# Performance work log

Hardware: AMD Instinct MI355X
Metric: run time of the kernel (lower is better)

## Reference

```python
import jax, jax.numpy as jnp
import numpy as np

B, V, C, M, CM, D, OUT = 16, 16, 64, 32, 16, 128, 600
VOCAB = {"cond": 4000, "proc": 2000, "drug": 600, "lab_item": 700, "lab_value": 2000, "inj_item": 400, "inj_value": 2000}


def _gru(x, Wih, Whh, bih, bhh):
    """Batch-first torch-style GRU. x: [N,T,D] -> (outputs [N,T,D], h_T [N,D])."""
    Dh = Whh.shape[1]

    def step(h, xt):
        gi = xt @ Wih.T + bih
        gh = h @ Whh.T + bhh
        ir, iz, ig = jnp.split(gi, 3, axis=-1)
        hr, hz, hg = jnp.split(gh, 3, axis=-1)
        r = jax.nn.sigmoid(ir + hr)
        z = jax.nn.sigmoid(iz + hz)
        n = jnp.tanh(ig + r * hg)
        h = (1.0 - z) * n + z * h
        return h, h

    h0 = jnp.zeros((x.shape[0], Dh), x.dtype)
    hT, ys = jax.lax.scan(step, h0, jnp.swapaxes(x, 0, 1))
    return jnp.swapaxes(ys, 0, 1), hT


def _hetero_mp(feats, Wself, Wmsg):
    """Heterogeneous message passing over node types on the fully-connected
    monitor<->visit-feature bipartite pattern: each node type combines a self
    transform with a transformed mean of the other node types, then ReLU.
    feats: list of [N,D]; Wself/Wmsg: [T,D,D]."""
    stacked = jnp.stack(feats)  # [T,N,D]
    total = jnp.sum(stacked, axis=0)
    T = stacked.shape[0]
    outs = []
    for t in range(T):
        others = (total - stacked[t]) / (T - 1)
        outs.append(jax.nn.relu(stacked[t] @ Wself[t] + others @ Wmsg[t]))
    return outs


def _forward(codes_cond, codes_proc, codes_drug, codes_lab_item, codes_lab_value,
             codes_inj_item, codes_inj_value, weight, age,
             emb_cond, emb_proc, emb_drug, emb_lab_item, emb_lab_value,
             emb_inj_item, emb_inj_value,
             mgru_Wih, mgru_Whh, mgru_bih, mgru_bhh,
             vgru_Wih, vgru_Whh, vgru_bih, vgru_bhh,
             gnn_Wself, gnn_Wmsg,
             fc_weight_W, fc_weight_b, fc_age_W, fc_age_b,
             fc_patient_W, fc_patient_b):
    # ---- visit-event features: embedding lookup + sum-pool over codes ----
    vis = {}
    for k, codes, emb in (("cond", codes_cond, emb_cond),
                          ("proc", codes_proc, emb_proc),
                          ("drug", codes_drug, emb_drug)):
        vis[k] = jnp.sum(emb[codes], axis=2)  # [B,V,D]
    visit_keys = ("cond", "proc", "drug")

    # ---- monitor-event pairs: (item * value) embeddings, GNN, two-level GRU ----
    pairs = (
        (codes_lab_item, codes_lab_value, emb_lab_item, emb_lab_value, "lab_item", (0, 2, 3, 4)),
        (codes_inj_item, codes_inj_value, emb_inj_item, emb_inj_value, "inj_item", (1, 2, 3, 4)),
    )
    hid = {}
    for p, (ci, cv, ei, ev, ikey, gidx) in enumerate(pairs):
        mon = jnp.sum(ei[ci] * ev[cv], axis=3)  # [B,V,M,D]
        feats = [mon.reshape(-1, D)]  # monitor node type, [B*V*M, D]
        for k in visit_keys:  # visit features repeated across monitors
            feats.append(jnp.broadcast_to(vis[k][:, :, None, :], (B, V, M, D)).reshape(-1, D))
        outs = _hetero_mp(feats, gnn_Wself[p], gnn_Wmsg[p])
        for t, k in enumerate((ikey,) + visit_keys):
            g = gidx[t]
            # monitor-level GRU over the M monitors of each visit
            o, _ = _gru(outs[t].reshape(B * V, M, D), mgru_Wih[g], mgru_Whh[g], mgru_bih[g], mgru_bhh[g])
            last = o[:, -1, :].reshape(B, V, D)  # last monitor state per visit
            # visit-level GRU (source uses visit_gru[feature_key1] for all keys)
            _, h = _gru(last, vgru_Wih[p], vgru_Whh[p], vgru_bih[p], vgru_bhh[p])
            hid[k] = h if k not in hid else hid[k] + h

    # ---- weight / age scalar features ----
    for k, x, W, b, vi in (("weight", weight, fc_weight_W, fc_weight_b, 2),
                           ("age", age, fc_age_W, fc_age_b, 3)):
        mask = (x != 0.0)[..., None]  # [B,V,1]
        xe = (x[..., None] * W[:, 0] + b) * mask  # Linear(1->D) then zero-mask
        _, h = _gru(xe, vgru_Wih[vi], vgru_Whh[vi], vgru_bih[vi], vgru_bhh[vi])
        hid[k] = h

    # ---- concat in dict-insertion order, then ReLU + Linear head ----
    pe = jnp.concatenate([hid["lab_item"], hid["cond"], hid["proc"], hid["drug"],
                          hid["inj_item"], hid["weight"], hid["age"]], axis=-1)  # [B, 7D]
    return jax.nn.relu(pe) @ fc_patient_W.T + fc_patient_b  # [B, OUT]


def setup_inputs() -> dict:
    key = jax.random.key(0)
    ks = iter(jax.random.split(key, 64))

    def nrm(shape, s=0.1):
        return (jax.random.normal(next(ks), shape) * s).astype(jnp.float32)

    def emb_table(vsz):
        t = nrm((vsz, D), 1.0)
        return t.at[0].set(0.0)  # padding_idx=0 row is zero

    inp = {}
    inp["codes_cond"] = jax.random.randint(next(ks), (B, V, C), 0, VOCAB["cond"], dtype=jnp.int32)
    inp["codes_proc"] = jax.random.randint(next(ks), (B, V, C), 0, VOCAB["proc"], dtype=jnp.int32)
    inp["codes_drug"] = jax.random.randint(next(ks), (B, V, C), 0, VOCAB["drug"], dtype=jnp.int32)
    inp["codes_lab_item"] = jax.random.randint(next(ks), (B, V, M, CM), 0, VOCAB["lab_item"], dtype=jnp.int32)
    inp["codes_lab_value"] = jax.random.randint(next(ks), (B, V, M, CM), 0, VOCAB["lab_value"], dtype=jnp.int32)
    inp["codes_inj_item"] = jax.random.randint(next(ks), (B, V, M, CM), 0, VOCAB["inj_item"], dtype=jnp.int32)
    inp["codes_inj_value"] = jax.random.randint(next(ks), (B, V, M, CM), 0, VOCAB["inj_value"], dtype=jnp.int32)
    inp["weight"] = jax.random.uniform(next(ks), (B, V), minval=0.1, maxval=1.0, dtype=jnp.float32)
    inp["age"] = jax.random.uniform(next(ks), (B, V), minval=0.1, maxval=1.0, dtype=jnp.float32)
    inp["emb_cond"] = emb_table(VOCAB["cond"])
    inp["emb_proc"] = emb_table(VOCAB["proc"])
    inp["emb_drug"] = emb_table(VOCAB["drug"])
    inp["emb_lab_item"] = emb_table(VOCAB["lab_item"])
    inp["emb_lab_value"] = emb_table(VOCAB["lab_value"])
    inp["emb_inj_item"] = emb_table(VOCAB["inj_item"])
    inp["emb_inj_value"] = emb_table(VOCAB["inj_value"])
    inp["mgru_Wih"] = nrm((5, 3 * D, D))
    inp["mgru_Whh"] = nrm((5, 3 * D, D))
    inp["mgru_bih"] = nrm((5, 3 * D))
    inp["mgru_bhh"] = nrm((5, 3 * D))
    inp["vgru_Wih"] = nrm((4, 3 * D, D))
    inp["vgru_Whh"] = nrm((4, 3 * D, D))
    inp["vgru_bih"] = nrm((4, 3 * D))
    inp["vgru_bhh"] = nrm((4, 3 * D))
    inp["gnn_Wself"] = nrm((2, 4, D, D))
    inp["gnn_Wmsg"] = nrm((2, 4, D, D))
    inp["fc_weight_W"] = nrm((D, 1))
    inp["fc_weight_b"] = nrm((D,))
    inp["fc_age_W"] = nrm((D, 1))
    inp["fc_age_b"] = nrm((D,))
    inp["fc_patient_W"] = nrm((OUT, 7 * D))
    inp["fc_patient_b"] = nrm((OUT,))
    return inp


def reference(codes_cond, codes_proc, codes_drug, codes_lab_item, codes_lab_value,
              codes_inj_item, codes_inj_value, weight, age,
              emb_cond, emb_proc, emb_drug, emb_lab_item, emb_lab_value,
              emb_inj_item, emb_inj_value,
              mgru_Wih, mgru_Whh, mgru_bih, mgru_bhh,
              vgru_Wih, vgru_Whh, vgru_bih, vgru_bhh,
              gnn_Wself, gnn_Wmsg,
              fc_weight_W, fc_weight_b, fc_age_W, fc_age_b,
              fc_patient_W, fc_patient_b):
    return _forward(codes_cond, codes_proc, codes_drug, codes_lab_item, codes_lab_value,
                    codes_inj_item, codes_inj_value, weight, age,
                    emb_cond, emb_proc, emb_drug, emb_lab_item, emb_lab_value,
                    emb_inj_item, emb_inj_value,
                    mgru_Wih, mgru_Whh, mgru_bih, mgru_bhh,
                    vgru_Wih, vgru_Whh, vgru_bih, vgru_bhh,
                    gnn_Wself, gnn_Wmsg,
                    fc_weight_W, fc_weight_b, fc_age_W, fc_age_b,
                    fc_patient_W, fc_patient_b)
```

## Files before the change

### kernel.cpp

```cpp
#include <hip/hip_runtime.h>
#include <math.h>

#define B_   16
#define V_   16
#define C_   64
#define M_   32
#define CM_  16
#define D_   128
#define OUT_ 600
#define NSEQ 256
#define NROW 8192

typedef __attribute__((ext_vector_type(8))) short bf16x8;
typedef __attribute__((ext_vector_type(4))) short bf16x4;
typedef __attribute__((ext_vector_type(4))) float f32x4;

__device__ __forceinline__ unsigned short f2bf(float x) {
  union { float f; unsigned u; } v; v.f = x;
  unsigned r = v.u + 0x7fff + ((v.u >> 16) & 1);
  return (unsigned short)(r >> 16);
}
__device__ __forceinline__ float bf2f(short s) {
  union { unsigned u; float f; } v;
  v.u = ((unsigned)(unsigned short)s) << 16;
  return v.f;
}
__device__ __forceinline__ float fsig(float x)  { return __fdividef(1.f, 1.f + __expf(-x)); }
__device__ __forceinline__ float ftanh(float x) { return 1.f - 2.f*__fdividef(1.f, __expf(2.f*x) + 1.f); }

constexpr int OFF_VIS   = 0;
constexpr int OFF_VISB  = 98304;
constexpr int OFF_MONB  = 147456;
constexpr int OFF_TOTB  = 1196032;
constexpr int OFF_W12T  = 2244608;
constexpr int OFF_WIHB  = 2375680;
constexpr int OFF_WIHTV = 2498560;
constexpr int OFF_XE    = 2695168;
constexpr int OFF_GI    = 2760704;
constexpr int OFF_LAST  = 27926528;
constexpr int OFF_VH    = 29171712;

__global__ __launch_bounds__(256) void k_prepvis(
    const float* __restrict__ Wself, const float* __restrict__ Wmsg,
    const float* __restrict__ mWih,  const float* __restrict__ vWih,
    const float* __restrict__ wgt,   const float* __restrict__ age,
    const float* __restrict__ fwW,   const float* __restrict__ fwB,
    const float* __restrict__ faW,   const float* __restrict__ faB,
    const int* __restrict__ cc, const int* __restrict__ cp, const int* __restrict__ cd,
    const float* __restrict__ ec, const float* __restrict__ ep, const float* __restrict__ ed,
    short* __restrict__ w12t, short* __restrict__ wihb,
    float* __restrict__ wihTv, float* __restrict__ xe,
    float* __restrict__ vis, short* __restrict__ visb)
{
  int bx = blockIdx.x, tid = threadIdx.x;
  if (bx < 1024) {
    int lin = bx*256 + tid;
    int pt = lin >> 15, rem = lin & 32767;
    int n = rem >> 8, k = rem & 255;
    float v;
    if (k < 128) v = Wself[pt*16384 + k*128 + n] - Wmsg[pt*16384 + k*128 + n]*(1.f/3.f);
    else         v = Wmsg[pt*16384 + (k-128)*128 + n]*(1.f/3.f);
    w12t[lin] = (short)f2bf(v);
  } else if (bx < 1984) {
    int lin = (bx-1024)*256 + tid;
    wihb[lin] = (short)f2bf(mWih[lin]);
  } else if (bx < 2752) {
    int lin = (bx-1984)*256 + tid;
    int g = lin / 49152, rem2 = lin % 49152;
    int k = rem2 / 384, j = rem2 % 384;
    wihTv[lin] = vWih[g*49152 + j*128 + k];
  } else if (bx < 3008) {
    int lin = (bx-2752)*256 + tid;
    int which = lin >> 15, rem2 = lin & 32767;
    int n = rem2 >> 7, d = rem2 & 127;
    float x  = which ? age[n] : wgt[n];
    float Wv = which ? faW[d] : fwW[d];
    float bb = which ? faB[d] : fwB[d];
    xe[lin] = (x != 0.0f) ? (x*Wv + bb) : 0.0f;
  } else {
    int idx = (bx-3008)*256 + tid;
    int type = idx >> 15;
    int r = idx & 32767;
    int bv = r >> 7, d = r & 127;
    const int*   codes = (type==0) ? cc : (type==1) ? cp : cd;
    const float* emb   = (type==0) ? ec : (type==1) ? ep : ed;
    float acc = 0.f;
    for (int c = 0; c < C_; ++c) {
      int code = codes[bv*C_ + c];
      acc += emb[code*D_ + d];
    }
    vis [(type*NSEQ + bv)*D_ + d] = acc;
    visb[(type*NSEQ + bv)*D_ + d] = (short)f2bf(acc);
  }
}

__global__ __launch_bounds__(128) void k_mon(
    const int* __restrict__ cli, const int* __restrict__ clv,
    const int* __restrict__ cii, const int* __restrict__ civ,
    const float* __restrict__ eli, const float* __restrict__ elv,
    const float* __restrict__ eii, const float* __restrict__ eiv,
    const float* __restrict__ vis,
    short* __restrict__ monb, short* __restrict__ totb)
{
  int p   = blockIdx.x >> 13;
  int bvm = blockIdx.x & 8191;
  int d   = threadIdx.x;
  const int* ci = p ? cii : cli;  const int* cv = p ? civ : clv;
  const float* ei = p ? eii : eli; const float* ev = p ? eiv : elv;
  float acc = 0.f;
  #pragma unroll
  for (int c = 0; c < CM_; ++c) {
    int iv = ci[bvm*CM_ + c];
    int vv = cv[bvm*CM_ + c];
    acc += ei[iv*D_ + d] * ev[vv*D_ + d];
  }
  int bv = bvm >> 5;
  float vsum = vis[bv*D_ + d] + vis[(NSEQ + bv)*D_ + d] + vis[(2*NSEQ + bv)*D_ + d];
  monb[(p*NROW + bvm)*D_ + d] = (short)f2bf(acc);
  totb[(p*NROW + bvm)*D_ + d] = (short)f2bf(acc + vsum);
}

__global__ __launch_bounds__(256, 4) void k_gg(
    const short* __restrict__ monb, const short* __restrict__ totb,
    const short* __restrict__ visb, const short* __restrict__ w12t,
    const short* __restrict__ wihb, const float* __restrict__ mbih,
    short* __restrict__ gi)
{
  const int pt = blockIdx.x >> 6;
  const int rb = blockIdx.x & 63;
  const int p = pt >> 2, t = pt & 3;
  const int g = (pt % 4 == 0) ? (pt / 4) : (pt % 4 + 1);
  const int row0 = rb * 128;
  const int tid = threadIdx.x;
  const int w = tid >> 6, lane = tid & 63;
  const int c = lane & 15, q = lane >> 4;

  __shared__ short smem[2*128*72];
  short (*Xs)[72]  = (short(*)[72])smem;
  short (*Ws)[72]  = (short(*)[72])(smem + 128*72);
  short (*Ys)[136] = (short(*)[136])smem;
  float (*giS)[68] = (float(*)[68])smem;

  const int rowL = tid >> 1, kc = tid & 1;
  const int rowG = row0 + rowL;
  const int bv = rowG >> 5;
  const int mg = w >> 1, ng = w & 1;

  f32x4 acc1[4][4];
  #pragma unroll
  for (int mi = 0; mi < 4; ++mi)
    #pragma unroll
    for (int ni = 0; ni < 4; ++ni) acc1[mi][ni] = (f32x4){0.f,0.f,0.f,0.f};

  const short* featp = (t == 0) ? (monb + ((size_t)p*NROW + rowG)*128)
                                : (visb + ((size_t)(t-1)*NSEQ + bv)*128);
  const short* totp  = totb + ((size_t)p*NROW + rowG)*128;
  const short* wrow  = w12t + ((size_t)pt*128 + rowL)*256;

  #pragma unroll 1
  for (int ks = 0; ks < 4; ++ks) {
    __syncthreads();
    int kg = ks*64 + kc*32;
    const short* srcX = (kg < 128) ? (featp + kg) : (totp + (kg - 128));
    const short* srcW = wrow + kg;
    short* dX = &Xs[rowL][kc*32];
    short* dW = &Ws[rowL][kc*32];
    #pragma unroll
    for (int i = 0; i < 4; ++i) {
      *(bf16x8*)(dX + 8*i) = *(const bf16x8*)(srcX + 8*i);
      *(bf16x8*)(dW + 8*i) = *(const bf16x8*)(srcW + 8*i);
    }
    __syncthreads();
    #pragma unroll
    for (int kk = 0; kk < 2; ++kk) {
      bf16x8 af[4], bfr[4];
      #pragma unroll
      for (int mi = 0; mi < 4; ++mi)
        af[mi] = *(const bf16x8*)&Xs[(mg*4+mi)*16 + c][kk*32 + q*8];
      #pragma unroll
      for (int ni = 0; ni < 4; ++ni)
        bfr[ni] = *(const bf16x8*)&Ws[(ng*4+ni)*16 + c][kk*32 + q*8];
      #pragma unroll
      for (int mi = 0; mi < 4; ++mi)
        #pragma unroll
        for (int ni = 0; ni < 4; ++ni)
          acc1[mi][ni] = __builtin_amdgcn_mfma_f32_16x16x32_bf16(af[mi], bfr[ni], acc1[mi][ni], 0, 0, 0);
    }
  }
  __syncthreads();

  #pragma unroll
  for (int mi = 0; mi < 4; ++mi)
    #pragma unroll
    for (int ni = 0; ni < 4; ++ni)
      #pragma unroll
      for (int reg = 0; reg < 4; ++reg)
        Ys[(mg*4+mi)*16 + q*4 + reg][(ng*4+ni)*16 + c] =
            (short)f2bf(fmaxf(acc1[mi][ni][reg], 0.f));
  __syncthreads();

  bf16x8 Af[2][4];
  #pragma unroll
  for (int mi = 0; mi < 2; ++mi)
    #pragma unroll
    for (int kt = 0; kt < 4; ++kt)
      Af[mi][kt] = *(const bf16x8*)&Ys[(w*2+mi)*16 + c][kt*32 + q*8];

  float bihv[24];
  #pragma unroll
  for (int nt = 0; nt < 24; ++nt)
    bihv[nt] = mbih[g*384 + nt*16 + c];

  short* gslab = gi + (((size_t)pt*64 + rb)*32)*384*4;
  #pragma unroll 1
  for (int cn = 0; cn < 6; ++cn) {
    f32x4 acc2[2][4];
    #pragma unroll
    for (int mi = 0; mi < 2; ++mi)
      #pragma unroll
      for (int ni = 0; ni < 4; ++ni) acc2[mi][ni] = (f32x4){0.f,0.f,0.f,0.f};
    #pragma unroll
    for (int ni = 0; ni < 4; ++ni) {
      int n = (cn*4 + ni)*16 + c;
      const short* bp_ = wihb + ((size_t)g*384 + n)*128 + q*8;
      #pragma unroll
      for (int kt = 0; kt < 4; ++kt) {
        bf16x8 bfr = *(const bf16x8*)(bp_ + kt*32);
        #pragma unroll
        for (int mi = 0; mi < 2; ++mi)
          acc2[mi][ni] = __builtin_amdgcn_mfma_f32_16x16x32_bf16(Af[mi][kt], bfr, acc2[mi][ni], 0, 0, 0);
      }
    }
    __syncthreads();
    #pragma unroll
    for (int mi = 0; mi < 2; ++mi)
      #pragma unroll
      for (int ni = 0; ni < 4; ++ni) {
        float bia = bihv[cn*4+ni];
        #pragma unroll
        for (int reg = 0; reg < 4; ++reg)
          giS[(w*2+mi)*16 + q*4 + reg][ni*16 + c] = acc2[mi][ni][reg] + bia;
      }
    __syncthreads();
    #pragma unroll
    for (int k = 0; k < 8; ++k) {
      int o4 = tid + k*256;
      int m = o4 >> 6, colL = o4 & 63;
      bf16x4 v;
      v[0] = (short)f2bf(giS[m][colL]);
      v[1] = (short)f2bf(giS[32+m][colL]);
      v[2] = (short)f2bf(giS[64+m][colL]);
      v[3] = (short)f2bf(giS[96+m][colL]);
      *(bf16x4*)&gslab[((size_t)m*384 + cn*64 + colL)*4] = v;
    }
  }
}

__global__ __launch_bounds__(512, 1) void k_mgru(
    const short* __restrict__ gi, const float* __restrict__ mWhh,
    const float* __restrict__ mbhh, float* __restrict__ last)
{
  const int run = blockIdx.x >> 5, grp = blockIdx.x & 31;
  const int g = (run % 4 == 0) ? (run / 4) : (run % 4 + 1);
  const int tid = threadIdx.x;
  const int w = tid >> 6;
  const int lane = tid & 63;
  const int c = lane & 15, q = lane >> 4;

  __shared__ short hb[2][4][16][40];
  for (int idx = tid; idx < 2*4*16*40; idx += 512)
    ((short*)hb)[idx] = 0;

  const int jh = w*16 + c;

  bf16x8 bfrag[3][4];
  #pragma unroll
  for (int gate = 0; gate < 3; ++gate) {
    const float* wp = mWhh + ((size_t)g*384 + gate*128 + jh)*128 + q*8;
    #pragma unroll
    for (int kt = 0; kt < 4; ++kt) {
      float4 lo = *(const float4*)(wp + kt*32);
      float4 hi = *(const float4*)(wp + kt*32 + 4);
      bf16x8 t;
      t[0]=(short)f2bf(lo.x); t[1]=(short)f2bf(lo.y); t[2]=(short)f2bf(lo.z); t[3]=(short)f2bf(lo.w);
      t[4]=(short)f2bf(hi.x); t[5]=(short)f2bf(hi.y); t[6]=(short)f2bf(hi.z); t[7]=(short)f2bf(hi.w);
      bfrag[gate][kt] = t;
    }
  }
  float bh_[3];
  #pragma unroll
  for (int gate = 0; gate < 3; ++gate)
    bh_[gate] = mbhh[g*384 + gate*128 + jh];

  float hf[4] = {0.f,0.f,0.f,0.f};
  const short* gib = gi + (((size_t)run*64 + grp*2 + q)*32)*384*4;
  const bool act = (lane < 32);

  bf16x4 gA[3], gB[3];
  if (act) {
    #pragma unroll
    for (int gate = 0; gate < 3; ++gate)
      gA[gate] = *(const bf16x4*)&gib[(size_t)(0*384 + gate*128 + jh)*4];
  }
  __syncthreads();

  auto dostep = [&](int m, bf16x4 (&gcur)[3], bf16x4 (&gnext)[3]) {
    const int cur = m & 1, nxt = cur ^ 1;
    bf16x8 a[4];
    #pragma unroll
    for (int kt = 0; kt < 4; ++kt)
      a[kt] = *(const bf16x8*)&hb[cur][kt][c][q*8];

    f32x4 acc[3];
    #pragma unroll
    for (int gate = 0; gate < 3; ++gate) {
      f32x4 t = {0.f,0.f,0.f,0.f};
      #pragma unroll
      for (int kt = 0; kt < 4; ++kt)
        t = __builtin_amdgcn_mfma_f32_16x16x32_bf16(a[kt], bfrag[gate][kt], t, 0, 0, 0);
      acc[gate] = t;
    }

    if (act && m < 31) {
      #pragma unroll
      for (int gate = 0; gate < 3; ++gate)
        gnext[gate] = *(const bf16x4*)&gib[(size_t)((m+1)*384 + gate*128 + jh)*4];
    }

    if (act) {
      const int kt = jh >> 5, kk = jh & 31;
      #pragma unroll
      for (int reg = 0; reg < 4; ++reg) {
        int row = q*4 + reg;
        float g0 = bf2f(gcur[0][reg]);
        float g1 = bf2f(gcur[1][reg]);
        float g2 = bf2f(gcur[2][reg]);
        float rr = fsig(acc[0][reg] + bh_[0] + g0);
        float zz = fsig(acc[1][reg] + bh_[1] + g1);
        float nn = ftanh(g2 + rr*(acc[2][reg] + bh_[2]));
        float hnew = (1.f - zz)*nn + zz*hf[reg];
        hf[reg] = hnew;
        hb[nxt][kt][row][kk] = (short)f2bf(hnew);
      }
    }
    __syncthreads();
  };

  #pragma unroll 1
  for (int m2 = 0; m2 < 16; ++m2) {
    dostep(2*m2,     gA, gB);
    dostep(2*m2 + 1, gB, gA);
  }

  if (act) {
    #pragma unroll
    for (int reg = 0; reg < 4; ++reg)
      last[(run*NSEQ + grp*8 + q*4 + reg)*D_ + jh] = hf[reg];
  }
}

__global__ __launch_bounds__(768) void k_vgru(
    const float* __restrict__ last, const float* __restrict__ xe,
    const float* __restrict__ wihTv, const float* __restrict__ vbih,
    const float* __restrict__ vWhh, const float* __restrict__ vbhh,
    float* __restrict__ vh)
{
  int run = blockIdx.x >> 4, b = blockIdx.x & 15;
  int tid = threadIdx.x;
  int vidx = (run < 4) ? 0 : (run < 8) ? 1 : (run - 6);

  __shared__ float Xs[16][128];
  __shared__ float giL[16*384];
  __shared__ __align__(16) float hsv[128];
  __shared__ float gh[384];

  const float* X = (run < 8) ? (last + ((size_t)run*NSEQ + b*16)*D_)
                             : (xe + ((size_t)(run-8)*NSEQ + b*16)*D_);
  for (int idx = tid; idx < 2048; idx += 768)
    ((float*)Xs)[idx] = X[idx];
  if (tid < 128) hsv[tid] = 0.f;
  __syncthreads();

  {
    int half = (tid >= 384) ? 1 : 0;
    int j = tid - half*384;
    float accv[8];
    float bias = vbih[vidx*384 + j];
    #pragma unroll
    for (int s = 0; s < 8; ++s) accv[s] = bias;
    const float* W = wihTv + vidx*49152 + j;
    #pragma unroll 4
    for (int k = 0; k < 128; ++k) {
      float wv = W[k*384];
      #pragma unroll
      for (int s = 0; s < 8; ++s) accv[s] += Xs[half*8 + s][k] * wv;
    }
    #pragma unroll
    for (int s = 0; s < 8; ++s)
      giL[(half*8 + s)*384 + j] = accv[s];
  }

  int j = tid >> 1, kh = tid & 1;
  float w[64];
  const float4* wrow = (const float4*)(vWhh + (vidx*384 + j)*128 + kh*64);
  #pragma unroll
  for (int k4 = 0; k4 < 16; ++k4) {
    float4 t4 = wrow[k4];
    w[4*k4] = t4.x; w[4*k4+1] = t4.y; w[4*k4+2] = t4.z; w[4*k4+3] = t4.w;
  }
  float bj = vbhh[vidx*384 + j];
  __syncthreads();

  #pragma unroll 1
  for (int v = 0; v < 16; ++v) {
    const float4* h4 = (const float4*)(hsv + kh*64);
    float p0 = 0.f, p1 = 0.f;
    #pragma unroll
    for (int k4 = 0; k4 < 8; ++k4) {
      float4 u0 = h4[k4], u1 = h4[k4+8];
      p0 += w[4*k4   ]*u0.x + w[4*k4+1 ]*u0.y + w[4*k4+2 ]*u0.z + w[4*k4+3 ]*u0.w;
      p1 += w[4*k4+32]*u1.x + w[4*k4+33]*u1.y + w[4*k4+34]*u1.z + w[4*k4+35]*u1.w;
    }
    float part = p0 + p1;
    part += __shfl_xor(part, 1);
    if (kh == 0) gh[j] = bj + ((j < 256) ? giL[v*384 + j] : 0.f) + part;
    __syncthreads();
    if (tid < 128) {
      float r = fsig(gh[tid]);
      float z = fsig(gh[tid+128]);
      float gin = giL[v*384 + 256 + tid];
      float n = ftanh(gin + r*gh[tid+256]);
      hsv[tid] = (1.f - z)*n + z*hsv[tid];
    }
    __syncthreads();
  }
  if (tid < 128) vh[(run*16 + b)*D_ + tid] = hsv[tid];
}

__global__ __launch_bounds__(256) void k_head(
    const float* __restrict__ vh, const float* __restrict__ Wp,
    const float* __restrict__ bp, float* __restrict__ out)
{
  const int o = blockIdx.x;
  const int tid = threadIdx.x;
  const int b = tid & 15, kc = tid >> 4;
  const int a1[7] = {0,1,2,3,4,8,9};
  const int a2[7] = {-1,5,6,7,-1,-1,-1};
  const float4* wb = (const float4*)(Wp + (size_t)o*896 + kc*56);
  float acc = 0.f;
  #pragma unroll
  for (int i = 0; i < 14; ++i) {
    int cc2 = kc*56 + i*4;
    int s = cc2 >> 7, d0 = cc2 & 127;
    float4 a = *(const float4*)(vh + (a1[s]*16 + b)*D_ + d0);
    int s2 = a2[s];
    if (s2 >= 0) {
      float4 a2v = *(const float4*)(vh + (s2*16 + b)*D_ + d0);
      a.x += a2v.x; a.y += a2v.y; a.z += a2v.z; a.w += a2v.w;
    }
    a.x = fmaxf(a.x, 0.f); a.y = fmaxf(a.y, 0.f);
    a.z = fmaxf(a.z, 0.f); a.w = fmaxf(a.w, 0.f);
    float4 ww = wb[i];
    acc += a.x*ww.x + a.y*ww.y + a.z*ww.z + a.w*ww.w;
  }
  __shared__ float red[16][17];
  red[kc][b] = acc;
  __syncthreads();
  if (tid < 16) {
    float s = 0.f;
    #pragma unroll
    for (int k = 0; k < 16; ++k) s += red[k][tid];
    out[tid*OUT_ + o] = s + bp[o];
  }
}

extern "C" void kernel_launch(void* const* d_in, const int* in_sizes, int n_in,
                              void* d_out, int out_size, void* d_ws, size_t ws_size,
                              hipStream_t stream)
{
  (void)in_sizes; (void)n_in; (void)out_size; (void)ws_size;
  const int*   cc   = (const int*)  d_in[0];
  const int*   cp   = (const int*)  d_in[1];
  const int*   cd   = (const int*)  d_in[2];
  const int*   cli  = (const int*)  d_in[3];
  const int*   clv  = (const int*)  d_in[4];
  const int*   cii  = (const int*)  d_in[5];
  const int*   civ  = (const int*)  d_in[6];
  const float* wgt  = (const float*)d_in[7];
  const float* age  = (const float*)d_in[8];
  const float* ec   = (const float*)d_in[9];
  const float* ep   = (const float*)d_in[10];
  const float* ed   = (const float*)d_in[11];
  const float* eli  = (const float*)d_in[12];
  const float* elv  = (const float*)d_in[13];
  const float* eii  = (const float*)d_in[14];
  const float* eiv  = (const float*)d_in[15];
  const float* mWih = (const float*)d_in[16];
  const float* mWhh = (const float*)d_in[17];
  const float* mbih = (const float*)d_in[18];
  const float* mbhh = (const float*)d_in[19];
  const float* vWih = (const float*)d_in[20];
  const float* vWhh = (const float*)d_in[21];
  const float* vbih = (const float*)d_in[22];
  const float* vbhh = (const float*)d_in[23];
  const float* Wself= (const float*)d_in[24];
  const float* Wmsg = (const float*)d_in[25];
  const float* fwW  = (const float*)d_in[26];
  const float* fwB  = (const float*)d_in[27];
  const float* faW  = (const float*)d_in[28];
  const float* faB  = (const float*)d_in[29];
  const float* Wp   = (const float*)d_in[30];
  const float* bp   = (const float*)d_in[31];
  float* out = (float*)d_out;
  float* ws  = (float*)d_ws;

  float* vis   = ws + OFF_VIS;
  short* visb  = (short*)(ws + OFF_VISB);
  short* monb  = (short*)(ws + OFF_MONB);
  short* totb  = (short*)(ws + OFF_TOTB);
  short* w12t  = (short*)(ws + OFF_W12T);
  short* wihb  = (short*)(ws + OFF_WIHB);
  float* wihTv = ws + OFF_WIHTV;
  float* xe    = ws + OFF_XE;
  short* gi    = (short*)(ws + OFF_GI);
  float* last  = ws + OFF_LAST;
  float* vh    = ws + OFF_VH;

  k_prepvis<<<3392, 256, 0, stream>>>(Wself, Wmsg, mWih, vWih, wgt, age,
                                      fwW, fwB, faW, faB,
                                      cc, cp, cd, ec, ep, ed,
                                      w12t, wihb, wihTv, xe, vis, visb);
  k_mon <<<16384, 128, 0, stream>>>(cli, clv, cii, civ, eli, elv, eii, eiv,
                                    vis, monb, totb);
  k_gg  <<<512, 256, 0, stream>>>(monb, totb, visb, w12t, wihb, mbih, gi);
  k_mgru<<<256, 512, 0, stream>>>(gi, mWhh, mbhh, last);
  k_vgru<<<160, 768, 0, stream>>>(last, xe, wihTv, vbih, vWhh, vbhh, vh);
  k_head<<<600, 256, 0, stream>>>(vh, Wp, bp, out);
}
```

Baseline: 279.7 us.

## Restructure monitor GRU to split MFMA and gate math across 1024-thread blocks

Result: no change. 280.8 us (+0.4%).

```diff
diff --git a/kernel.cpp b/kernel.cpp
--- a/kernel.cpp
+++ b/kernel.cpp
@@ -24,6 +24,9 @@
   union { unsigned u; float f; } v;
   v.u = ((unsigned)(unsigned short)s) << 16;
   return v.f;
+}
+__device__ __forceinline__ float u2f(unsigned u) {
+  union { unsigned u; float f; } v; v.u = u; return v.f;
 }
 __device__ __forceinline__ float fsig(float x)  { return __fdividef(1.f, 1.f + __expf(-x)); }
 __device__ __forceinline__ float ftanh(float x) { return 1.f - 2.f*__fdividef(1.f, __expf(2.f*x) + 1.f); }
@@ -256,11 +259,12 @@
   }
 }
 
-__global__ __launch_bounds__(512, 1) void k_mgru(
+__global__ __launch_bounds__(1024) void k_mgru(
     const short* __restrict__ gi, const float* __restrict__ mWhh,
     const float* __restrict__ mbhh, float* __restrict__ last)
 {
-  const int run = blockIdx.x >> 5, grp = blockIdx.x & 31;
+  const int run  = blockIdx.x >> 4;
+  const int pair = blockIdx.x & 15;
   const int g = (run % 4 == 0) ? (run / 4) : (run % 4 + 1);
   const int tid = threadIdx.x;
   const int w = tid >> 6;
@@ -268,95 +272,104 @@
   const int c = lane & 15, q = lane >> 4;
 
   __shared__ short hb[2][4][16][40];
-  for (int idx = tid; idx < 2*4*16*40; idx += 512)
+  __shared__ float gS[384][20];
+
+  for (int idx = tid; idx < 2*4*16*40; idx += 1024)
     ((short*)hb)[idx] = 0;
 
-  const int jh = w*16 + c;
-
-  bf16x8 bfrag[3][4];
-  #pragma unroll
-  for (int gate = 0; gate < 3; ++gate) {
-    const float* wp = mWhh + ((size_t)g*384 + gate*128 + jh)*128 + q*8;
-    #pragma unroll
-    for (int kt = 0; kt < 4; ++kt) {
-      float4 lo = *(const float4*)(wp + kt*32);
-      float4 hi = *(const float4*)(wp + kt*32 + 4);
-      bf16x8 t;
-      t[0]=(short)f2bf(lo.x); t[1]=(short)f2bf(lo.y); t[2]=(short)f2bf(lo.z); t[3]=(short)f2bf(lo.w);
-      t[4]=(short)f2bf(hi.x); t[5]=(short)f2bf(hi.y); t[6]=(short)f2bf(hi.z); t[7]=(short)f2bf(hi.w);
-      bfrag[gate][kt] = t;
-    }
-  }
-  float bh_[3];
+  const bool mfw = (w < 12);
+  const int gate_w = w >> 2;
+  const int nt = w & 3;
+  bf16x8 bfrag[2][4];
+  if (mfw) {
+    #pragma unroll
+    for (int ti = 0; ti < 2; ++ti) {
+      const int col = gate_w*128 + nt*32 + ti*16 + c;
+      const float* wp = mWhh + ((size_t)g*384 + col)*128 + q*8;
+      #pragma unroll
+      for (int kt = 0; kt < 4; ++kt) {
+        float4 lo = *(const float4*)(wp + kt*32);
+        float4 hi = *(const float4*)(wp + kt*32 + 4);
+        bf16x8 tt;
+        tt[0]=(short)f2bf(lo.x); tt[1]=(short)f2bf(lo.y); tt[2]=(short)f2bf(lo.z); tt[3]=(short)f2bf(lo.w);
+        tt[4]=(short)f2bf(hi.x); tt[5]=(short)f2bf(hi.y); tt[6]=(short)f2bf(hi.z); tt[7]=(short)f2bf(hi.w);
+        bfrag[ti][kt] = tt;
+      }
+    }
+  }
+
+  const int j  = tid >> 3;
+  const int sp = tid & 7;
+  const int s0 = sp*2;
+  const int ktj = j >> 5, kkj = j & 31;
+  const float bh0 = mbhh[g*384 +       j];
+  const float bh1 = mbhh[g*384 + 128 + j];
+  const float bh2 = mbhh[g*384 + 256 + j];
+  const short* gip = gi + (((size_t)run*64 + pair*4 + (s0>>2))*32)*384*4
+                        + (size_t)j*4 + (s0&3);
+
+  float h0 = 0.f, h1 = 0.f;
+
+  unsigned gA[3], gB[3];
   #pragma unroll
   for (int gate = 0; gate < 3; ++gate)
-    bh_[gate] = mbhh[g*384 + gate*128 + jh];
-
-  float hf[4] = {0.f,0.f,0.f,0.f};
-  const short* gib = gi + (((size_t)run*64 + grp*2 + q)*32)*384*4;
-  const bool act = (lane < 32);
-
-  bf16x4 gA[3], gB[3];
-  if (act) {
-    #pragma unroll
-    for (int gate = 0; gate < 3; ++gate)
-      gA[gate] = *(const bf16x4*)&gib[(size_t)(0*384 + gate*128 + jh)*4];
-  }
+    gA[gate] = *(const unsigned*)(gip + gate*512);
   __syncthreads();
 
-  auto dostep = [&](int m, bf16x4 (&gcur)[3], bf16x4 (&gnext)[3]) {
+  auto step = [&](int m, unsigned (&gcur)[3], unsigned (&gnext)[3]) {
     const int cur = m & 1, nxt = cur ^ 1;
-    bf16x8 a[4];
-    #pragma unroll
-    for (int kt = 0; kt < 4; ++kt)
-      a[kt] = *(const bf16x8*)&hb[cur][kt][c][q*8];
-
-    f32x4 acc[3];
-    #pragma unroll
-    for (int gate = 0; gate < 3; ++gate) {
-      f32x4 t = {0.f,0.f,0.f,0.f};
+    if (mfw) {
+      bf16x8 a[4];
       #pragma unroll
       for (int kt = 0; kt < 4; ++kt)
-        t = __builtin_amdgcn_mfma_f32_16x16x32_bf16(a[kt], bfrag[gate][kt], t, 0, 0, 0);
-      acc[gate] = t;
-    }
-
-    if (act && m < 31) {
+        a[kt] = *(const bf16x8*)&hb[cur][kt][c][q*8];
+      #pragma unroll
+      for (int ti = 0; ti < 2; ++ti) {
+        f32x4 acc = (f32x4){0.f,0.f,0.f,0.f};
+        #pragma unroll
+        for (int kt = 0; kt < 4; ++kt)
+          acc = __builtin_amdgcn_mfma_f32_16x16x32_bf16(a[kt], bfrag[ti][kt], acc, 0, 0, 0);
+        const int col = gate_w*128 + nt*32 + ti*16 + c;
+        *(f32x4*)&gS[col][q*4] = acc;
+      }
+    }
+    __syncthreads();
+
+    float2 vr = *(const float2*)&gS[      j][s0];
+    float2 vz = *(const float2*)&gS[128 + j][s0];
+    float2 vn = *(const float2*)&gS[256 + j][s0];
+    if (m < 31) {
+      const short* gp = gip + (size_t)(m+1)*1536;
       #pragma unroll
       for (int gate = 0; gate < 3; ++gate)
-        gnext[gate] = *(const bf16x4*)&gib[(size_t)((m+1)*384 + gate*128 + jh)*4];
-    }
-
-    if (act) {
-      const int kt = jh >> 5, kk = jh & 31;
-      #pragma unroll
-      for (int reg = 0; reg < 4; ++reg) {
-        int row = q*4 + reg;
-        float g0 = bf2f(gcur[0][reg]);
-        float g1 = bf2f(gcur[1][reg]);
-        float g2 = bf2f(gcur[2][reg]);
-        float rr = fsig(acc[0][reg] + bh_[0] + g0);
-        float zz = fsig(acc[1][reg] + bh_[1] + g1);
-        float nn = ftanh(g2 + rr*(acc[2][reg] + bh_[2]));
-        float hnew = (1.f - zz)*nn + zz*hf[reg];
-        hf[reg] = hnew;
-        hb[nxt][kt][row][kk] = (short)f2bf(hnew);
-      }
-    }
+        gnext[gate] = *(const unsigned*)(gp + gate*512);
+    }
+    float gi0a = u2f(gcur[0] << 16), gi0b = u2f(gcur[0] & 0xffff0000u);
+    float gi1a = u2f(gcur[1] << 16), gi1b = u2f(gcur[1] & 0xffff0000u);
+    float gi2a = u2f(gcur[2] << 16), gi2b = u2f(gcur[2] & 0xffff0000u);
+
+    float r0 = fsig(vr.x + bh0 + gi0a);
+    float z0 = fsig(vz.x + bh1 + gi1a);
+    float n0 = ftanh(gi2a + r0*(vn.x + bh2));
+    h0 = (1.f - z0)*n0 + z0*h0;
+    float r1 = fsig(vr.y + bh0 + gi0b);
+    float z1 = fsig(vz.y + bh1 + gi1b);
+    float n1 = ftanh(gi2b + r1*(vn.y + bh2));
+    h1 = (1.f - z1)*n1 + z1*h1;
+
+    hb[nxt][ktj][s0    ][kkj] = (short)f2bf(h0);
+    hb[nxt][ktj][s0 + 1][kkj] = (short)f2bf(h1);
     __syncthreads();
   };
 
   #pragma unroll 1
   for (int m2 = 0; m2 < 16; ++m2) {
-    dostep(2*m2,     gA, gB);
-    dostep(2*m2 + 1, gB, gA);
-  }
-
-  if (act) {
-    #pragma unroll
-    for (int reg = 0; reg < 4; ++reg)
-      last[(run*NSEQ + grp*8 + q*4 + reg)*D_ + jh] = hf[reg];
-  }
+    step(2*m2,     gA, gB);
+    step(2*m2 + 1, gB, gA);
+  }
+
+  last[((size_t)run*NSEQ + pair*16 + s0    )*D_ + j] = h0;
+  last[((size_t)run*NSEQ + pair*16 + s0 + 1)*D_ + j] = h1;
 }
 
 __global__ __launch_bounds__(768) void k_vgru(
@@ -533,7 +546,7 @@
   k_mon <<<16384, 128, 0, stream>>>(cli, clv, cii, civ, eli, elv, eii, eiv,
                                     vis, monb, totb);
   k_gg  <<<512, 256, 0, stream>>>(monb, totb, visb, w12t, wihb, mbih, gi);
-  k_mgru<<<256, 512, 0, stream>>>(gi, mWhh, mbhh, last);
+  k_mgru<<<128, 1024, 0, stream>>>(gi, mWhh, mbhh, last);
   k_vgru<<<160, 768, 0, stream>>>(last, xe, wihTv, vbih, vWhh, vbhh, vh);
   k_head<<<600, 256, 0, stream>>>(vh, Wp, bp, out);
 }
```

## Pack 16 sequences per monitor-GRU block using all MFMA rows

Applied to the files above, without the earlier changes.

New measurement: 268.7 us. 1.04x faster.

```diff
diff --git a/kernel.cpp b/kernel.cpp
--- a/kernel.cpp
+++ b/kernel.cpp
@@ -25,8 +25,17 @@
   v.u = ((unsigned)(unsigned short)s) << 16;
   return v.f;
 }
+__device__ __forceinline__ float u2f(unsigned u) {
+  union { unsigned u; float f; } v; v.u = u; return v.f;
+}
 __device__ __forceinline__ float fsig(float x)  { return __fdividef(1.f, 1.f + __expf(-x)); }
 __device__ __forceinline__ float ftanh(float x) { return 1.f - 2.f*__fdividef(1.f, __expf(2.f*x) + 1.f); }
+
+__device__ __forceinline__ void ldsbar() {
+  asm volatile("s_waitcnt lgkmcnt(0)" ::: "memory");
+  __builtin_amdgcn_s_barrier();
+  asm volatile("" ::: "memory");
+}
 
 constexpr int OFF_VIS   = 0;
 constexpr int OFF_VISB  = 98304;
@@ -256,27 +265,28 @@
   }
 }
 
-__global__ __launch_bounds__(512, 1) void k_mgru(
+__global__ __launch_bounds__(512, 2) void k_mgru(
     const short* __restrict__ gi, const float* __restrict__ mWhh,
     const float* __restrict__ mbhh, float* __restrict__ last)
 {
-  const int run = blockIdx.x >> 5, grp = blockIdx.x & 31;
+  const int run  = blockIdx.x >> 4;
+  const int pair = blockIdx.x & 15;
   const int g = (run % 4 == 0) ? (run / 4) : (run % 4 + 1);
   const int tid = threadIdx.x;
   const int w = tid >> 6;
   const int lane = tid & 63;
   const int c = lane & 15, q = lane >> 4;
+  const int j = w*16 + c;
 
   __shared__ short hb[2][4][16][40];
+
   for (int idx = tid; idx < 2*4*16*40; idx += 512)
     ((short*)hb)[idx] = 0;
 
-  const int jh = w*16 + c;
-
   bf16x8 bfrag[3][4];
   #pragma unroll
   for (int gate = 0; gate < 3; ++gate) {
-    const float* wp = mWhh + ((size_t)g*384 + gate*128 + jh)*128 + q*8;
+    const float* wp = mWhh + ((size_t)g*384 + gate*128 + j)*128 + q*8;
     #pragma unroll
     for (int kt = 0; kt < 4; ++kt) {
       float4 lo = *(const float4*)(wp + kt*32);
@@ -287,30 +297,28 @@
       bfrag[gate][kt] = t;
     }
   }
-  float bh_[3];
+  const float bh0 = mbhh[g*384 +       j];
+  const float bh1 = mbhh[g*384 + 128 + j];
+  const float bh2 = mbhh[g*384 + 256 + j];
+
+  const short* gib = gi + ((size_t)((run*64 + pair*4 + q)*32))*1536;
+
+  float hf[4] = {0.f,0.f,0.f,0.f};
+  const int ktw = w >> 1;
+  const int kkw = (w & 1)*16 + c;
+
+  bf16x4 gA[3], gB[3];
   #pragma unroll
   for (int gate = 0; gate < 3; ++gate)
-    bh_[gate] = mbhh[g*384 + gate*128 + jh];
-
-  float hf[4] = {0.f,0.f,0.f,0.f};
-  const short* gib = gi + (((size_t)run*64 + grp*2 + q)*32)*384*4;
-  const bool act = (lane < 32);
-
-  bf16x4 gA[3], gB[3];
-  if (act) {
-    #pragma unroll
-    for (int gate = 0; gate < 3; ++gate)
-      gA[gate] = *(const bf16x4*)&gib[(size_t)(0*384 + gate*128 + jh)*4];
-  }
+    gA[gate] = *(const bf16x4*)&gib[(size_t)(gate*128 + j)*4];
   __syncthreads();
 
-  auto dostep = [&](int m, bf16x4 (&gcur)[3], bf16x4 (&gnext)[3]) {
+  auto step = [&](int m, bf16x4 (&gcur)[3], bf16x4 (&gnext)[3]) {
     const int cur = m & 1, nxt = cur ^ 1;
     bf16x8 a[4];
     #pragma unroll
     for (int kt = 0; kt < 4; ++kt)
       a[kt] = *(const bf16x8*)&hb[cur][kt][c][q*8];
-
     f32x4 acc[3];
     #pragma unroll
     for (int gate = 0; gate < 3; ++gate) {
@@ -320,43 +328,36 @@
         t = __builtin_amdgcn_mfma_f32_16x16x32_bf16(a[kt], bfrag[gate][kt], t, 0, 0, 0);
       acc[gate] = t;
     }
-
-    if (act && m < 31) {
+    if (m < 31) {
+      const short* gp = gib + (size_t)(m+1)*1536;
       #pragma unroll
       for (int gate = 0; gate < 3; ++gate)
-        gnext[gate] = *(const bf16x4*)&gib[(size_t)((m+1)*384 + gate*128 + jh)*4];
-    }
-
-    if (act) {
-      const int kt = jh >> 5, kk = jh & 31;
-      #pragma unroll
-      for (int reg = 0; reg < 4; ++reg) {
-        int row = q*4 + reg;
-        float g0 = bf2f(gcur[0][reg]);
-        float g1 = bf2f(gcur[1][reg]);
-        float g2 = bf2f(gcur[2][reg]);
-        float rr = fsig(acc[0][reg] + bh_[0] + g0);
-        float zz = fsig(acc[1][reg] + bh_[1] + g1);
-        float nn = ftanh(g2 + rr*(acc[2][reg] + bh_[2]));
-        float hnew = (1.f - zz)*nn + zz*hf[reg];
-        hf[reg] = hnew;
-        hb[nxt][kt][row][kk] = (short)f2bf(hnew);
-      }
-    }
-    __syncthreads();
+        gnext[gate] = *(const bf16x4*)&gp[(size_t)(gate*128 + j)*4];
+    }
+    #pragma unroll
+    for (int reg = 0; reg < 4; ++reg) {
+      float g0 = bf2f(gcur[0][reg]);
+      float g1 = bf2f(gcur[1][reg]);
+      float g2 = bf2f(gcur[2][reg]);
+      float rr = fsig(acc[0][reg] + bh0 + g0);
+      float zz = fsig(acc[1][reg] + bh1 + g1);
+      float nn = ftanh(g2 + rr*(acc[2][reg] + bh2));
+      float hnew = (1.f - zz)*nn + zz*hf[reg];
+      hf[reg] = hnew;
+      hb[nxt][ktw][q*4 + reg][kkw] = (short)f2bf(hnew);
+    }
+    ldsbar();
   };
 
   #pragma unroll 1
   for (int m2 = 0; m2 < 16; ++m2) {
-    dostep(2*m2,     gA, gB);
-    dostep(2*m2 + 1, gB, gA);
-  }
-
-  if (act) {
-    #pragma unroll
-    for (int reg = 0; reg < 4; ++reg)
-      last[(run*NSEQ + grp*8 + q*4 + reg)*D_ + jh] = hf[reg];
-  }
+    step(2*m2,     gA, gB);
+    step(2*m2 + 1, gB, gA);
+  }
+
+  #pragma unroll
+  for (int reg = 0; reg < 4; ++reg)
+    last[((size_t)run*NSEQ + pair*16 + q*4 + reg)*D_ + j] = hf[reg];
 }
 
 __global__ __launch_bounds__(768) void k_vgru(
@@ -533,7 +534,7 @@
   k_mon <<<16384, 128, 0, stream>>>(cli, clv, cii, civ, eli, elv, eii, eiv,
                                     vis, monb, totb);
   k_gg  <<<512, 256, 0, stream>>>(monb, totb, visb, w12t, wihb, mbih, gi);
-  k_mgru<<<256, 512, 0, stream>>>(gi, mWhh, mbhh, last);
+  k_mgru<<<128, 512, 0, stream>>>(gi, mWhh, mbhh, last);
   k_vgru<<<160, 768, 0, stream>>>(last, xe, wihTv, vbih, vWhh, vbhh, vh);
   k_head<<<600, 256, 0, stream>>>(vh, Wp, bp, out);
 }
```
